# Performance work log

Hardware: AMD Instinct MI355X
Metric: run time of the kernel (lower is better)

The kernel has to match this reference:

```python
import jax, jax.numpy as jnp
import numpy as np
import math

N_HEADS = 16
FACTOR = 5
EPS = 1e-5


def layernorm(x, g, b):
    m = x.mean(-1, keepdims=True)
    v = x.var(-1, keepdims=True)
    return (x - m) / jnp.sqrt(v + EPS) * g + b


def prob_attention(Q, K, V, mask_flag, key):
    # Q: [B, L_Q, H, D], K/V: [B, L_K, H, D] -> internal [B, H, L, D] (Informer ProbAttention)
    Q = Q.transpose(0, 2, 1, 3)
    K = K.transpose(0, 2, 1, 3)
    V = V.transpose(0, 2, 1, 3)
    B, H, L_Q, D = Q.shape
    L_K = K.shape[2]
    U_part = min(FACTOR * int(np.ceil(np.log(L_K))), L_K)  # sampled keys per query
    u = min(FACTOR * int(np.ceil(np.log(L_Q))), L_Q)       # number of active queries
    # sample U_part key indices per query (shared over B, H as in Informer)
    idx = jax.random.randint(key, (L_Q, U_part), 0, L_K)
    K_s = K[:, :, idx, :]                                   # [B,H,L_Q,U_part,D]
    QKs = jnp.einsum('bhld,bhlsd->bhls', Q, K_s)            # sampled scores
    M = QKs.max(-1) - QKs.sum(-1) / L_K                     # sparsity measurement [B,H,L_Q]
    M_top = jax.lax.top_k(M, u)[1]                          # [B,H,u] active query indices
    Q_r = jnp.take_along_axis(Q, M_top[..., None], axis=2)  # [B,H,u,D]
    scale = 1.0 / math.sqrt(D)
    scores = jnp.einsum('bhud,bhkd->bhuk', Q_r, K) * scale  # [B,H,u,L_K]
    if mask_flag:
        # causal mask relative to each selected query's position
        causal = jnp.arange(L_K)[None, None, None, :] > M_top[..., None]
        scores = jnp.where(causal, -jnp.inf, scores)
        context = jnp.cumsum(V, axis=2)                     # initial context for masked case
    else:
        context = jnp.broadcast_to(V.mean(axis=2, keepdims=True), (B, H, L_Q, D))
    attn = jax.nn.softmax(scores, axis=-1)
    ctx = jnp.einsum('bhuk,bhkd->bhud', attn, V)            # [B,H,u,D]
    bi = jnp.arange(B)[:, None, None]
    hi = jnp.arange(H)[None, :, None]
    context = context.at[bi, hi, M_top].set(ctx)            # scatter active queries
    return context.transpose(0, 2, 1, 3)                    # [B,L_Q,H,D]


def mha(x, kv, Wq, bq, Wk, bk, Wv, bv, Wo, bo, mask_flag, key):
    B, L, Dm = x.shape
    Lc = kv.shape[1]
    Dh = Dm // N_HEADS
    Q = (x @ Wq + bq).reshape(B, L, N_HEADS, Dh)
    K = (kv @ Wk + bk).reshape(B, Lc, N_HEADS, Dh)
    V = (kv @ Wv + bv).reshape(B, Lc, N_HEADS, Dh)
    out = prob_attention(Q, K, V, mask_flag, key).reshape(B, L, Dm)
    return out @ Wo + bo


def forward(x, enc_out, sa_Wq, sa_bq, sa_Wk, sa_bk, sa_Wv, sa_bv, sa_Wo, sa_bo,
            ca_Wq, ca_bq, ca_Wk, ca_bk, ca_Wv, ca_bv, ca_Wo, ca_bo,
            ln1_g, ln1_b, ln2_g, ln2_b, ln3_g, ln3_b, ff_W1, ff_b1, ff_W2, ff_b2):
    k1, k2 = jax.random.split(jax.random.key(42))
    x2 = mha(x, x, sa_Wq, sa_bq, sa_Wk, sa_bk, sa_Wv, sa_bv, sa_Wo, sa_bo, True, k1)
    x = layernorm(x + x2, ln1_g, ln1_b)
    x2 = mha(x, enc_out, ca_Wq, ca_bq, ca_Wk, ca_bk, ca_Wv, ca_bv, ca_Wo, ca_bo, False, k2)
    x = layernorm(x + x2, ln2_g, ln2_b)
    x2 = (jax.nn.relu(x @ ff_W1 + ff_b1)) @ ff_W2 + ff_b2
    return layernorm(x + x2, ln3_g, ln3_b)


def setup_inputs() -> dict:
    key = jax.random.key(0)
    D, F = 1024, 4096
    B, L = 4, 1024
    ks = jax.random.split(key, 16)
    s = 0.02
    inp = {
        'x': jax.random.normal(ks[0], (B, L, D), jnp.float32),
        'enc_out': jax.random.normal(ks[1], (B, L, D), jnp.float32),
    }
    names = ['sa_Wq', 'sa_Wk', 'sa_Wv', 'sa_Wo', 'ca_Wq', 'ca_Wk', 'ca_Wv', 'ca_Wo']
    for i, n in enumerate(names):
        inp[n] = jax.random.normal(ks[2 + i], (D, D), jnp.float32) * s
        inp[n.replace('W', 'b')] = jnp.zeros((D,), jnp.float32)
    inp['ff_W1'] = jax.random.normal(ks[10], (D, F), jnp.float32) * s
    inp['ff_b1'] = jnp.zeros((F,), jnp.float32)
    inp['ff_W2'] = jax.random.normal(ks[11], (F, D), jnp.float32) * s
    inp['ff_b2'] = jnp.zeros((D,), jnp.float32)
    for i in (1, 2, 3):
        inp[f'ln{i}_g'] = jnp.ones((D,), jnp.float32)
        inp[f'ln{i}_b'] = jnp.zeros((D,), jnp.float32)
    return inp


def reference(x, enc_out, sa_Wq, sa_bq, sa_Wk, sa_bk, sa_Wv, sa_bv, sa_Wo, sa_bo,
              ca_Wq, ca_bq, ca_Wk, ca_bk, ca_Wv, ca_bv, ca_Wo, ca_bo,
              ln1_g, ln1_b, ln2_g, ln2_b, ln3_g, ln3_b, ff_W1, ff_b1, ff_W2, ff_b2):
    return forward(x, enc_out, sa_Wq, sa_bq, sa_Wk, sa_bk, sa_Wv, sa_bv, sa_Wo, sa_bo,
                   ca_Wq, ca_bq, ca_Wk, ca_bk, ca_Wv, ca_bv, ca_Wo, ca_bo,
                   ln1_g, ln1_b, ln2_g, ln2_b, ln3_g, ln3_b, ff_W1, ff_b1, ff_W2, ff_b2)
```

## Files before the change

kernel.cpp:

```cpp
#include <hip/hip_runtime.h>
#include <cstdint>
#include <cstddef>

#define B_     4
#define L_     1024
#define DM_    1024
#define H_     16
#define DH_    64
#define U_     35
#define FF_    4096
#define MROWS_ 4096
#define IDXN_  35840
#define KSC_   16
#define KSP_   16

typedef __attribute__((ext_vector_type(8))) short bf16x8;
typedef __attribute__((ext_vector_type(4))) float f32x4;

__host__ __device__ inline void tf2x32(uint32_t k0, uint32_t k1,
                                       uint32_t x0, uint32_t x1,
                                       uint32_t& y0, uint32_t& y1) {
  const uint32_t ks2 = k0 ^ k1 ^ 0x1BD11BDAu;
  uint32_t v0 = x0 + k0, v1 = x1 + k1;
#define ROTL_(x,d) (((x)<<(d))|((x)>>(32-(d))))
#define RND_(r) { v0 += v1; v1 = ROTL_(v1,(r)); v1 ^= v0; }
  RND_(13) RND_(15) RND_(26) RND_(6)   v0 += k1;  v1 += ks2 + 1u;
  RND_(17) RND_(29) RND_(16) RND_(24)  v0 += ks2; v1 += k0  + 2u;
  RND_(13) RND_(15) RND_(26) RND_(6)   v0 += k0;  v1 += k1  + 3u;
  RND_(17) RND_(29) RND_(16) RND_(24)  v0 += k1;  v1 += ks2 + 4u;
  RND_(13) RND_(15) RND_(26) RND_(6)   v0 += ks2; v1 += k0  + 5u;
#undef RND_
#undef ROTL_
  y0 = v0; y1 = v1;
}

__global__ void idx_kernel(uint32_t k0, uint32_t k1, int* __restrict__ idx) {
  const int i = blockIdx.x * 256 + threadIdx.x;
  if (i >= IDXN_) return;
  uint32_t y0, y1;
  tf2x32(k0, k1, 0u, (uint32_t)i, y0, y1);
  idx[i] = (int)((y0 ^ y1) & 1023u);
}

__device__ __forceinline__ uint32_t f32bits(float x) {
  union { float f; uint32_t u; } c; c.f = x; return c.u;
}
__device__ __forceinline__ float bitsf32(uint32_t u) {
  union { uint32_t u; float f; } c; c.u = u; return c.f;
}
__device__ __forceinline__ uint32_t bf16rne(float x) {
  const uint32_t u = f32bits(x);
  return (u + 0x7FFFu + ((u >> 16) & 1u)) >> 16;
}
__device__ __forceinline__ float bf16tof(uint32_t h) { return bitsf32(h << 16); }

__device__ __forceinline__ void split3(float x, uint32_t& h, uint32_t& m, uint32_t& l) {
  h = bf16rne(x); const float r  = x - bf16tof(h);
  m = bf16rne(r); const float r2 = r - bf16tof(m);
  l = bf16rne(r2);
}

__device__ __forceinline__ void gload16(const void* g, void* l) {
  __builtin_amdgcn_global_load_lds(
      (const __attribute__((address_space(1))) void*)g,
      (__attribute__((address_space(3))) void*)l, 16, 0, 0);
}

struct TSJob { const float* W; short* Th; short* Tm; short* Tl; int K; int N; int limbs; int nblk; };
struct TSJobs { TSJob j[4]; int cnt; };

__global__ __launch_bounds__(256) void tsplit_batch(TSJobs jobs)
{
  __shared__ float tile[64][65];
  int local = blockIdx.x;
  int ji = 0;
  while (ji < jobs.cnt - 1 && local >= jobs.j[ji].nblk) { local -= jobs.j[ji].nblk; ++ji; }
  const TSJob J = jobs.j[ji];
  const int ntiles = J.N >> 6;
  const int n0 = (local % ntiles) * 64;
  const int k0 = (local / ntiles) * 64;

  const int t = threadIdx.x;
  const int r = t >> 2, c0 = (t & 3) * 16;
  const float* src = J.W + (size_t)(k0 + r) * J.N + n0 + c0;
  const float4 v0 = *(const float4*)src;
  const float4 v1 = *(const float4*)(src + 4);
  const float4 v2 = *(const float4*)(src + 8);
  const float4 v3 = *(const float4*)(src + 12);
  float* tr = &tile[r][c0];
  tr[0]=v0.x; tr[1]=v0.y; tr[2]=v0.z; tr[3]=v0.w;
  tr[4]=v1.x; tr[5]=v1.y; tr[6]=v1.z; tr[7]=v1.w;
  tr[8]=v2.x; tr[9]=v2.y; tr[10]=v2.z; tr[11]=v2.w;
  tr[12]=v3.x; tr[13]=v3.y; tr[14]=v3.z; tr[15]=v3.w;
  __syncthreads();
  uint32_t ph[8], pm[8], pl[8];
#pragma unroll
  for (int j = 0; j < 16; j += 2) {
    uint32_t h0,m0,l0,h1,m1,l1;
    split3(tile[c0 + j][r], h0, m0, l0);
    split3(tile[c0 + j + 1][r], h1, m1, l1);
    ph[j>>1] = h0 | (h1 << 16);
    pm[j>>1] = m0 | (m1 << 16);
    pl[j>>1] = l0 | (l1 << 16);
  }
  const size_t ob = (size_t)(n0 + r) * J.K + k0 + c0;
  *(uint4*)(J.Th + ob)     = make_uint4(ph[0], ph[1], ph[2], ph[3]);
  *(uint4*)(J.Th + ob + 8) = make_uint4(ph[4], ph[5], ph[6], ph[7]);
  if (J.limbs == 3) {
    *(uint4*)(J.Tm + ob)     = make_uint4(pm[0], pm[1], pm[2], pm[3]);
    *(uint4*)(J.Tm + ob + 8) = make_uint4(pm[4], pm[5], pm[6], pm[7]);
    *(uint4*)(J.Tl + ob)     = make_uint4(pl[0], pl[1], pl[2], pl[3]);
    *(uint4*)(J.Tl + ob + 8) = make_uint4(pl[4], pl[5], pl[6], pl[7]);
  }
}

template<int LIMBS>
__global__ void rsplit_kernel(const float* __restrict__ X, short* __restrict__ Th,
                              short* __restrict__ Tm, short* __restrict__ Tl, int n8)
{
  const int i = blockIdx.x * 256 + threadIdx.x;
  if (i >= n8) return;
  const float4 a = ((const float4*)X)[2*i], b = ((const float4*)X)[2*i+1];
  const float v[8] = {a.x,a.y,a.z,a.w,b.x,b.y,b.z,b.w};
  uint32_t ph[4], pm[4], pl[4];
#pragma unroll
  for (int j = 0; j < 4; ++j) {
    uint32_t h0,m0,l0,h1,m1,l1;
    split3(v[2*j], h0, m0, l0);
    split3(v[2*j+1], h1, m1, l1);
    ph[j] = h0 | (h1 << 16); pm[j] = m0 | (m1 << 16); pl[j] = l0 | (l1 << 16);
  }
  ((uint4*)Th)[i] = make_uint4(ph[0], ph[1], ph[2], ph[3]);
  if (LIMBS == 3) {
    ((uint4*)Tm)[i] = make_uint4(pm[0], pm[1], pm[2], pm[3]);
    ((uint4*)Tl)[i] = make_uint4(pl[0], pl[1], pl[2], pl[3]);
  }
}

struct FJob {
  const short* A[3];
  const short* B[3];
  const float* bias;
  float* C;
  short* Ch;
  int relu;
};
struct FJobs { FJob j[3]; };

template<int NL>
__global__ __launch_bounds__(256, 3) void gemm_fused(FJobs jobs, int K, int N)
{
  __shared__ short As[NL][4096] __attribute__((aligned(16)));
  __shared__ short Bs[NL][4096] __attribute__((aligned(16)));
  const int z = blockIdx.z;
  const int nwg  = gridDim.x * gridDim.y;
  const int flat = blockIdx.y * gridDim.x + blockIdx.x;
  const int swz  = (flat & 7) * (nwg >> 3) + (flat >> 3);
  const int bn = (swz % gridDim.x) * 128;
  const int bm = (swz / gridDim.x) * 128;

  const int t = threadIdx.x, lane = t & 63;
  const int wid = t >> 6, wr = wid >> 1, wc = wid & 1;
  const int l15 = lane & 15, kg = lane >> 4;
  const int srow = t >> 2;
  const int sc   = ((t & 3) ^ ((srow + (srow >> 2)) & 3)) * 8;

  int aoff[4], boff[4];
#pragma unroll
  for (int m = 0; m < 4; ++m) {
    const int ra = wr * 64 + m * 16 + l15;
    aoff[m] = ra * 32 + ((kg ^ ((ra + (ra >> 2)) & 3)) << 3);
    const int rb = wc * 64 + m * 16 + l15;
    boff[m] = rb * 32 + ((kg ^ ((rb + (rb >> 2)) & 3)) << 3);
  }

  f32x4 acc[4][4];
#pragma unroll
  for (int m = 0; m < 4; ++m)
#pragma unroll
    for (int n = 0; n < 4; ++n) acc[m][n] = (f32x4){0.f,0.f,0.f,0.f};

  const size_t aofs0 = (size_t)(bm + srow) * K + sc;
  const size_t bofs0 = (size_t)(bn + srow) * K + sc;
  const size_t half  = (size_t)64 * K;

  for (int kk = 0; kk < K; kk += 32) {
    __syncthreads();
#pragma unroll
    for (int l = 0; l < NL; ++l) {
      gload16(jobs.j[z].A[l] + aofs0 + kk,        &As[l][t * 8]);
      gload16(jobs.j[z].A[l] + aofs0 + half + kk, &As[l][2048 + t * 8]);
      gload16(jobs.j[z].B[l] + bofs0 + kk,        &Bs[l][t * 8]);
      gload16(jobs.j[z].B[l] + bofs0 + half + kk, &Bs[l][2048 + t * 8]);
    }
    __syncthreads();
    if (NL == 1) {
      bf16x8 a[4], b[4];
#pragma unroll
      for (int m = 0; m < 4; ++m) a[m] = *(const bf16x8*)&As[0][aoff[m]];
#pragma unroll
      for (int n = 0; n < 4; ++n) b[n] = *(const bf16x8*)&Bs[0][boff[n]];
#pragma unroll
      for (int m = 0; m < 4; ++m)
#pragma unroll
        for (int n = 0; n < 4; ++n)
          acc[m][n] = __builtin_amdgcn_mfma_f32_16x16x32_bf16(a[m], b[n], acc[m][n], 0, 0, 0);
    } else {
      bf16x8 a0[4], a1[4], a2[4], b[4];
#pragma unroll
      for (int m = 0; m < 4; ++m) {
        a0[m] = *(const bf16x8*)&As[0][aoff[m]];
        a1[m] = *(const bf16x8*)&As[1][aoff[m]];
        a2[m] = *(const bf16x8*)&As[2][aoff[m]];
      }
#pragma unroll
      for (int n = 0; n < 4; ++n) b[n] = *(const bf16x8*)&Bs[0][boff[n]];
#pragma unroll
      for (int m = 0; m < 4; ++m)
#pragma unroll
        for (int n = 0; n < 4; ++n) {
          acc[m][n] = __builtin_amdgcn_mfma_f32_16x16x32_bf16(a0[m], b[n], acc[m][n], 0, 0, 0);
          acc[m][n] = __builtin_amdgcn_mfma_f32_16x16x32_bf16(a1[m], b[n], acc[m][n], 0, 0, 0);
          acc[m][n] = __builtin_amdgcn_mfma_f32_16x16x32_bf16(a2[m], b[n], acc[m][n], 0, 0, 0);
        }
#pragma unroll
      for (int n = 0; n < 4; ++n) b[n] = *(const bf16x8*)&Bs[1][boff[n]];
#pragma unroll
      for (int m = 0; m < 4; ++m)
#pragma unroll
        for (int n = 0; n < 4; ++n) {
          acc[m][n] = __builtin_amdgcn_mfma_f32_16x16x32_bf16(a0[m], b[n], acc[m][n], 0, 0, 0);
          acc[m][n] = __builtin_amdgcn_mfma_f32_16x16x32_bf16(a1[m], b[n], acc[m][n], 0, 0, 0);
        }
#pragma unroll
      for (int n = 0; n < 4; ++n) b[n] = *(const bf16x8*)&Bs[2][boff[n]];
#pragma unroll
      for (int m = 0; m < 4; ++m)
#pragma unroll
        for (int n = 0; n < 4; ++n)
          acc[m][n] = __builtin_amdgcn_mfma_f32_16x16x32_bf16(a0[m], b[n], acc[m][n], 0, 0, 0);
    }
  }

  const float* bias = jobs.j[z].bias;
  float* C  = jobs.j[z].C;
  short* Ch = jobs.j[z].Ch;
  const int relu = jobs.j[z].relu;
  float bv[4];
#pragma unroll
  for (int n = 0; n < 4; ++n) bv[n] = bias[bn + wc*64 + n*16 + l15];
#pragma unroll
  for (int m = 0; m < 4; ++m) {
    const int row0 = bm + wr*64 + m*16 + kg*4;
#pragma unroll
    for (int n = 0; n < 4; ++n) {
      const int col = bn + wc*64 + n*16 + l15;
#pragma unroll
      for (int q = 0; q < 4; ++q) {
        float o = acc[m][n][q] + bv[n];
        if (relu) o = fmaxf(o, 0.f);
        const size_t off = (size_t)(row0 + q) * N + col;
        if (C)  C[off]  = o;
        if (Ch) Ch[off] = (short)bf16rne(o);
      }
    }
  }
}

__global__ __launch_bounds__(256, 3) void gemm_one(FJob job, int K, int N)
{
  __shared__ short As[2][4096] __attribute__((aligned(16)));
  __shared__ short Bs[2][4096] __attribute__((aligned(16)));
  const int nwg  = gridDim.x * gridDim.y;
  const int flat = blockIdx.y * gridDim.x + blockIdx.x;
  const int swz  = (flat & 7) * (nwg >> 3) + (flat >> 3);
  const int bn = (swz % gridDim.x) * 128;
  const int bm = (swz / gridDim.x) * 128;

  const int t = threadIdx.x, lane = t & 63;
  const int wid = t >> 6, wr = wid >> 1, wc = wid & 1;
  const int l15 = lane & 15, kg = lane >> 4;
  const int srow = t >> 2;
  const int sc   = ((t & 3) ^ ((srow + (srow >> 2)) & 3)) * 8;

  int aoff[4], boff[4];
#pragma unroll
  for (int m = 0; m < 4; ++m) {
    const int ra = wr * 64 + m * 16 + l15;
    aoff[m] = ra * 32 + ((kg ^ ((ra + (ra >> 2)) & 3)) << 3);
    const int rb = wc * 64 + m * 16 + l15;
    boff[m] = rb * 32 + ((kg ^ ((rb + (rb >> 2)) & 3)) << 3);
  }

  f32x4 acc[4][4];
#pragma unroll
  for (int m = 0; m < 4; ++m)
#pragma unroll
    for (int n = 0; n < 4; ++n) acc[m][n] = (f32x4){0.f,0.f,0.f,0.f};

  const size_t aofs0 = (size_t)(bm + srow) * K + sc;
  const size_t bofs0 = (size_t)(bn + srow) * K + sc;
  const size_t half  = (size_t)64 * K;

  gload16(job.A[0] + aofs0,        &As[0][t * 8]);
  gload16(job.A[0] + aofs0 + half, &As[0][2048 + t * 8]);
  gload16(job.B[0] + bofs0,        &Bs[0][t * 8]);
  gload16(job.B[0] + bofs0 + half, &Bs[0][2048 + t * 8]);
  __syncthreads();

  int cur = 0;
  for (int kk = 0; kk < K; kk += 32) {
    const int nxt = kk + 32;
    if (nxt < K) {
      const int nb = cur ^ 1;
      gload16(job.A[0] + aofs0 + nxt,        &As[nb][t * 8]);
      gload16(job.A[0] + aofs0 + half + nxt, &As[nb][2048 + t * 8]);
      gload16(job.B[0] + bofs0 + nxt,        &Bs[nb][t * 8]);
      gload16(job.B[0] + bofs0 + half + nxt, &Bs[nb][2048 + t * 8]);
    }
    bf16x8 a[4], b[4];
#pragma unroll
    for (int m = 0; m < 4; ++m) a[m] = *(const bf16x8*)&As[cur][aoff[m]];
#pragma unroll
    for (int n = 0; n < 4; ++n) b[n] = *(const bf16x8*)&Bs[cur][boff[n]];
#pragma unroll
    for (int m = 0; m < 4; ++m)
#pragma unroll
      for (int n = 0; n < 4; ++n)
        acc[m][n] = __builtin_amdgcn_mfma_f32_16x16x32_bf16(a[m], b[n], acc[m][n], 0, 0, 0);
    __syncthreads();
    cur ^= 1;
  }

  const float* bias = job.bias;
  float* C  = job.C;
  short* Ch = job.Ch;
  const int relu = job.relu;
  float bv[4];
#pragma unroll
  for (int n = 0; n < 4; ++n) bv[n] = bias[bn + wc*64 + n*16 + l15];
#pragma unroll
  for (int m = 0; m < 4; ++m) {
    const int row0 = bm + wr*64 + m*16 + kg*4;
#pragma unroll
    for (int n = 0; n < 4; ++n) {
      const int col = bn + wc*64 + n*16 + l15;
#pragma unroll
      for (int q = 0; q < 4; ++q) {
        float o = acc[m][n][q] + bv[n];
        if (relu) o = fmaxf(o, 0.f);
        const size_t off = (size_t)(row0 + q) * N + col;
        if (C)  C[off]  = o;
        if (Ch) Ch[off] = (short)bf16rne(o);
      }
    }
  }
}

__global__ __launch_bounds__(256, 2) void qks_m_kernel(
    const float* __restrict__ Q, const float* __restrict__ K,
    const int* __restrict__ idx, float* __restrict__ Mout)
{
  __shared__ int sidx[64 * U_];
  const int p = blockIdx.x;
  const int g  = (p & 7) + (((p >> 3) & 7) << 3);
  const int q16 = p >> 6;
  const int l0 = q16 * 64;
  const int tid = threadIdx.x;
  for (int i = tid; i < 64 * U_; i += 256) sidx[i] = idx[l0 * U_ + i];
  __syncthreads();

  const int ll = tid >> 2, dq = tid & 3;
  const int l = l0 + ll;
  const int h = g & (H_ - 1), b = g >> 4;
  const size_t rowb = (size_t)(b * L_) * DM_ + h * DH_;
  const float* qrow = Q + rowb + (size_t)l * DM_ + dq * 4;
  float4 qv[4];
#pragma unroll
  for (int jj = 0; jj < 4; ++jj) qv[jj] = *(const float4*)(qrow + jj * 16);

  const int* ip = &sidx[ll * U_];
  float mx = -__builtin_inff();
  float sm = 0.f;
#pragma unroll 5
  for (int s = 0; s < U_; ++s) {
    const float* krow = K + rowb + (size_t)ip[s] * DM_ + dq * 4;
    const float4 k0 = *(const float4*)(krow);
    const float4 k1 = *(const float4*)(krow + 16);
    const float4 k2 = *(const float4*)(krow + 32);
    const float4 k3 = *(const float4*)(krow + 48);
    float a0 = 0.f, a1 = 0.f, a2 = 0.f, a3 = 0.f;
    a0 = fmaf(qv[0].x, k0.x, a0); a0 = fmaf(qv[0].y, k0.y, a0);
    a0 = fmaf(qv[0].z, k0.z, a0); a0 = fmaf(qv[0].w, k0.w, a0);
    a1 = fmaf(qv[1].x, k1.x, a1); a1 = fmaf(qv[1].y, k1.y, a1);
    a1 = fmaf(qv[1].z, k1.z, a1); a1 = fmaf(qv[1].w, k1.w, a1);
    a2 = fmaf(qv[2].x, k2.x, a2); a2 = fmaf(qv[2].y, k2.y, a2);
    a2 = fmaf(qv[2].z, k2.z, a2); a2 = fmaf(qv[2].w, k2.w, a2);
    a3 = fmaf(qv[3].x, k3.x, a3); a3 = fmaf(qv[3].y, k3.y, a3);
    a3 = fmaf(qv[3].z, k3.z, a3); a3 = fmaf(qv[3].w, k3.w, a3);
    float a = (a0 + a1) + (a2 + a3);
    a += __shfl_xor(a, 1, 64);
    a += __shfl_xor(a, 2, 64);
    mx = fmaxf(mx, a);
    sm += a;
  }
  if (dq == 0) Mout[g * L_ + l] = mx - sm * (1.0f / 1024.0f);
}

__global__ __launch_bounds__(256) void topk_kernel(
    const float* __restrict__ M, int* __restrict__ Mtop)
{
  const int bh  = blockIdx.x;
  const int tid = threadIdx.x;
  __shared__ float vals[L_];
  __shared__ float rv[256];
  __shared__ int   ri[256];
  for (int i = tid; i < L_; i += 256) vals[i] = M[(size_t)bh * L_ + i];
  __syncthreads();
  for (int t = 0; t < U_; ++t) {
    float best = -__builtin_inff();
    int   bi   = L_;
    for (int i = tid; i < L_; i += 256) {
      const float v = vals[i];
      if (v > best) { best = v; bi = i; }
    }
    rv[tid] = best; ri[tid] = bi;
    __syncthreads();
    for (int s = 128; s > 0; s >>= 1) {
      if (tid < s) {
        if (rv[tid+s] > rv[tid] || (rv[tid+s] == rv[tid] && ri[tid+s] < ri[tid])) {
          rv[tid] = rv[tid+s]; ri[tid] = ri[tid+s];
        }
      }
      __syncthreads();
    }
    if (tid == 0) { Mtop[bh * U_ + t] = ri[0]; vals[ri[0]] = -__builtin_inff(); }
    __syncthreads();
  }
}

__global__ __launch_bounds__(256) void attn_score(
    const float* __restrict__ Q, const float* __restrict__ K,
    const int* __restrict__ Mtop, uint32_t* __restrict__ Pg, int masked)
{
  __shared__ float qs[U_ * DH_];
  __shared__ int   rowsL[U_ + 1];
  const int p = blockIdx.x;
  const int xcd = p & 7, idx2 = p >> 3;
  const int bh = xcd + ((idx2 & 7) << 3);
  const int ks = idx2 >> 3;
  const int h = bh & (H_ - 1), b = bh >> 4;
  const int tid = threadIdx.x;
  const size_t kvbase = (size_t)(b * L_) * DM_ + h * DH_;

  if (tid < U_) rowsL[tid] = Mtop[bh * U_ + tid];
  __syncthreads();
  for (int i = tid; i < U_ * DH_; i += 256)
    qs[i] = Q[kvbase + (size_t)rowsL[i >> 6] * DM_ + (i & 63)];
  __syncthreads();

  const int grp = tid >> 2, dq = tid & 3;
  const int k = ks * 64 + grp;
  const float* kp = K + kvbase + (size_t)k * DM_ + dq * 16;
  const float4 kv0 = *(const float4*)(kp);
  const float4 kv1 = *(const float4*)(kp + 4);
  const float4 kv2 = *(const float4*)(kp + 8);
  const float4 kv3 = *(const float4*)(kp + 12);

#define DOT_EXP_U(uu, out)                                                  \
  {                                                                         \
    const float4* qp = (const float4*)&qs[(uu) * 64 + dq * 16];             \
    const float4 q0 = qp[0], q1 = qp[1], q2 = qp[2], q3 = qp[3];            \
    float x0 = 0.f, x1 = 0.f;                                               \
    x0 = fmaf(q0.x, kv0.x, x0); x0 = fmaf(q0.y, kv0.y, x0);                 \
    x0 = fmaf(q0.z, kv0.z, x0); x0 = fmaf(q0.w, kv0.w, x0);                 \
    x1 = fmaf(q1.x, kv1.x, x1); x1 = fmaf(q1.y, kv1.y, x1);                 \
    x1 = fmaf(q1.z, kv1.z, x1); x1 = fmaf(q1.w, kv1.w, x1);                 \
    x0 = fmaf(q2.x, kv2.x, x0); x0 = fmaf(q2.y, kv2.y, x0);                 \
    x0 = fmaf(q2.z, kv2.z, x0); x0 = fmaf(q2.w, kv2.w, x0);                 \
    x1 = fmaf(q3.x, kv3.x, x1); x1 = fmaf(q3.y, kv3.y, x1);                 \
    x1 = fmaf(q3.z, kv3.z, x1); x1 = fmaf(q3.w, kv3.w, x1);                 \
    float a = x0 + x1;                                                      \
    a += __shfl_xor(a, 1, 64);                                              \
    a += __shfl_xor(a, 2, 64);                                              \
    float v = a * 0.125f;                                                   \
    if (masked && k > rowsL[(uu)]) v = -__builtin_inff();                   \
    out = expf(v);                                                          \
  }

  uint32_t pk[18];
#pragma unroll
  for (int j = 0; j < 17; ++j) {
    float e0, e1;
    DOT_EXP_U(2 * j, e0);
    DOT_EXP_U(2 * j + 1, e1);
    pk[j] = bf16rne(e0) | (bf16rne(e1) << 16);
  }
  {
    float e;
    DOT_EXP_U(34, e);
    pk[17] = bf16rne(e);
  }
#undef DOT_EXP_U

  if (dq == 0) {
    uint32_t* prow = Pg + (size_t)bh * (L_ * 18) + (size_t)k * 18;
#pragma unroll
    for (int j = 0; j < 18; ++j) prow[j] = pk[j];
  }
}

__global__ __launch_bounds__(256) void attn_pv(
    const float* __restrict__ V, const uint32_t* __restrict__ Pg,
    float* __restrict__ Opart, float* __restrict__ Dpart)
{
  __shared__ uint32_t Pl[64 * 18];
  const int p = blockIdx.x;
  const int xcd = p & 7, idx2 = p >> 3;
  const int bh = xcd + ((idx2 & 7) << 3);
  const int ks = idx2 >> 3;
  const int h = bh & (H_ - 1), b = bh >> 4;
  const int tid = threadIdx.x, lane = tid & 63, wid = tid >> 6;
  const size_t kvbase = (size_t)(b * L_) * DM_ + h * DH_;

  const uint32_t* ps = Pg + (size_t)bh * (L_ * 18) + (size_t)(ks * 64) * 18;
  for (int i = tid; i < 64 * 18; i += 256) Pl[i] = ps[i];
  __syncthreads();

  float acc[9], dd[9];
#pragma unroll
  for (int j = 0; j < 9; ++j) { acc[j] = 0.f; dd[j] = 0.f; }

  const float* vp = V + kvbase + (size_t)(ks * 64) * DM_ + lane;
  const int widh = wid >> 1;
  const int hi   = wid & 1;
#pragma unroll 8
  for (int kk = 0; kk < 64; ++kk) {
    const float v0 = vp[(size_t)kk * DM_];
    const uint32_t* pr = &Pl[kk * 18];
#pragma unroll
    for (int j = 0; j < 9; ++j) {
      if (wid + 4 * j < U_) {
        const uint32_t w = pr[widh + 2 * j];
        const float p2 = hi ? bitsf32(w & 0xFFFF0000u) : bitsf32(w << 16);
        acc[j] = fmaf(p2, v0, acc[j]);
        dd[j] += p2;
      }
    }
  }
  const int pb = (ks * 64 + bh) * U_;
#pragma unroll
  for (int j = 0; j < 9; ++j) {
    const int u = wid + 4 * j;
    if (u < U_) {
      Opart[(size_t)(pb + u) * 64 + lane] = acc[j];
      if (lane == 0) Dpart[pb + u] = dd[j];
    }
  }
}

__global__ void attn_reduce(const float* __restrict__ Opart,
                            const float* __restrict__ Dpart,
                            float* __restrict__ ctx_rows)
{
  const int bhu = blockIdx.x;
  const int bh = bhu / U_, u = bhu % U_;
  const int lane = threadIdx.x;
  float o = 0.f, dd = 0.f;
#pragma unroll
  for (int ks = 0; ks < KSP_; ++ks) {
    o  += Opart[(size_t)((ks * 64 + bh) * U_ + u) * 64 + lane];
    dd += Dpart[(ks * 64 + bh) * U_ + u];
  }
  ctx_rows[(size_t)bhu * 64 + lane] = o / dd;
}

__global__ __launch_bounds__(256) void cumsum_kernel(
    const float* __restrict__ V, float* __restrict__ C)
{
  const int bh = blockIdx.x;
  const int h = bh & (H_ - 1), b = bh >> 4;
  const int d = threadIdx.x & 63, qq = threadIdx.x >> 6;
  __shared__ float chs[4][DH_];
  const size_t base = (size_t)b * L_ * DM_ + h * DH_ + d;
  float acc = 0.f;
  const int l0 = qq * 256;
  for (int l = l0; l < l0 + 256; ++l) acc += V[base + (size_t)l * DM_];
  chs[qq][d] = acc;
  __syncthreads();
  float off = 0.f;
  for (int j = 0; j < qq; ++j) off += chs[j][d];
  acc = off;
  for (int l = l0; l < l0 + 256; ++l) {
    acc += V[base + (size_t)l * DM_];
    C[base + (size_t)l * DM_] = acc;
  }
}

__global__ __launch_bounds__(256) void vmean_kernel(
    const float* __restrict__ V, float* __restrict__ vm)
{
  const int bh = blockIdx.x;
  const int h = bh & (H_ - 1), b = bh >> 4;
  const int d = threadIdx.x & 63, qq = threadIdx.x >> 6;
  __shared__ float chs[4][DH_];
  const size_t base = (size_t)b * L_ * DM_ + h * DH_ + d;
  float acc = 0.f;
  for (int l = qq * 256; l < qq * 256 + 256; ++l) acc += V[base + (size_t)l * DM_];
  chs[qq][d] = acc;
  __syncthreads();
  if (qq == 0)
    vm[bh * DH_ + d] = (chs[0][d] + chs[1][d] + chs[2][d] + chs[3][d]) * (1.0f / 1024.0f);
}

__global__ void fill_kernel(const float* __restrict__ vm, float* __restrict__ C)
{
  const size_t i = (size_t)blockIdx.x * 256 + threadIdx.x;
  const int d = (int)(i & 63);
  const int h = (int)((i >> 6) & (H_ - 1));
  const int b = (int)(i >> 20);
  C[i] = vm[(b * H_ + h) * DH_ + d];
}

__global__ void scatter_kernel(const float* __restrict__ ctx_rows,
                               const int* __restrict__ Mtop, float* __restrict__ C)
{
  const int bhu = blockIdx.x;
  const int u  = bhu % U_;
  const int bh = bhu / U_;
  const int h = bh & (H_ - 1), b = bh >> 4;
  const int row = Mtop[bh * U_ + u];
  C[(size_t)(b * L_ + row) * DM_ + h * DH_ + threadIdx.x] =
      ctx_rows[(size_t)bhu * DH_ + threadIdx.x];
}

__global__ __launch_bounds__(256) void ln_kernel(
    const float* __restrict__ xa, const float* __restrict__ xb,
    const float* __restrict__ g, const float* __restrict__ bt,
    float* __restrict__ out, short* __restrict__ oh,
    short* __restrict__ om, short* __restrict__ ol)
{
  const int row = blockIdx.x;
  const int tid = threadIdx.x;
  __shared__ float v[DM_];
  __shared__ float red[256];
  float s = 0.f;
  for (int i = tid; i < DM_; i += 256) {
    const float t = xa[(size_t)row * DM_ + i] + xb[(size_t)row * DM_ + i];
    v[i] = t; s += t;
  }
  red[tid] = s; __syncthreads();
  for (int st = 128; st > 0; st >>= 1) { if (tid < st) red[tid] += red[tid+st]; __syncthreads(); }
  const float mean = red[0] * (1.0f / DM_);
  __syncthreads();
  float s2 = 0.f;
  for (int i = tid; i < DM_; i += 256) { const float dd = v[i] - mean; s2 += dd * dd; }
  red[tid] = s2; __syncthreads();
  for (int st = 128; st > 0; st >>= 1) { if (tid < st) red[tid] += red[tid+st]; __syncthreads(); }
  const float rstd = rsqrtf(red[0] * (1.0f / DM_) + 1e-5f);
  __syncthreads();
  for (int i = tid; i < DM_; i += 256) {
    const size_t idx = (size_t)row * DM_ + i;
    const float o = (v[i] - mean) * rstd * g[i] + bt[i];
    out[idx] = o;
    if (oh) {
      const uint32_t h = bf16rne(o);
      oh[idx] = (short)h;
      if (om) {
        const float r = o - bf16tof(h);
        const uint32_t m = bf16rne(r);
        om[idx] = (short)m;
        ol[idx] = (short)bf16rne(r - bf16tof(m));
      }
    }
  }
}

extern "C" void kernel_launch(void* const* d_in, const int* in_sizes, int n_in,
                              void* d_out, int out_size, void* d_ws, size_t ws_size,
                              hipStream_t stream)
{
  (void)in_sizes; (void)n_in; (void)out_size; (void)ws_size;
  const float* x    = (const float*)d_in[0];
  const float* enc  = (const float*)d_in[1];
  const float* saWq = (const float*)d_in[2];  const float* sabq = (const float*)d_in[3];
  const float* saWk = (const float*)d_in[4];  const float* sabk = (const float*)d_in[5];
  const float* saWv = (const float*)d_in[6];  const float* sabv = (const float*)d_in[7];
  const float* saWo = (const float*)d_in[8];  const float* sabo = (const float*)d_in[9];
  const float* caWq = (const float*)d_in[10]; const float* cabq = (const float*)d_in[11];
  const float* caWk = (const float*)d_in[12]; const float* cabk = (const float*)d_in[13];
  const float* caWv = (const float*)d_in[14]; const float* cabv = (const float*)d_in[15];
  const float* caWo = (const float*)d_in[16]; const float* cabo = (const float*)d_in[17];
  const float* fW1  = (const float*)d_in[18]; const float* fb1  = (const float*)d_in[19];
  const float* fW2  = (const float*)d_in[20]; const float* fb2  = (const float*)d_in[21];
  const float* l1g  = (const float*)d_in[22]; const float* l1b  = (const float*)d_in[23];
  const float* l2g  = (const float*)d_in[24]; const float* l2b  = (const float*)d_in[25];
  const float* l3g  = (const float*)d_in[26]; const float* l3b  = (const float*)d_in[27];

  float* ws = (float*)d_ws;
  const size_t SL = (size_t)MROWS_ * DM_;
  float* bufQ = ws;
  float* bufK = ws + SL;
  float* bufV = ws + 2 * SL;
  float* bufC = ws + 3 * SL;
  float* xcur = ws + 4 * SL;
  float* tmp  = ws + 5 * SL;
  float* smallp = ws + 6 * SL;
  int*   idxb = (int*)smallp;
  float* Mbuf = smallp + 36864;
  int*   Mtop = (int*)(smallp + 36864 + 65536);
  float* ctxr = smallp + 36864 + 65536 + 2304;
  float* vm   = ctxr + 143360;

  uint32_t* Pg    = (uint32_t*)bufC;
  float*    Opart = bufC + 1179648;
  float*    Dpart = Opart + (size_t)KSP_ * 64 * U_ * 64;

  const size_t M1 = 1024u * 1024u;
  short* wreg = (short*)(ws + 6 * SL + 262144);
  short* areg = wreg + 8 * M1;
  short* Wqh = wreg;          short* Wqm = wreg + 1*M1; short* Wql = wreg + 2*M1;
  short* Wkh = wreg + 3*M1;   short* Wkm = wreg + 4*M1; short* Wkl = wreg + 5*M1;
  short* Wvh = wreg + 6*M1;   short* Woh = wreg + 7*M1;
  short* f1h = wreg;          short* f2h = wreg + 4*M1;
  short* xh = areg;           short* xm = areg + 4*M1;  short* xl = areg + 8*M1;
  short* eh = areg + 12*M1;   short* em = areg + 16*M1; short* el = areg + 20*M1;
  short* bCh = areg + 12*M1;
  short* hidh = (short*)bufQ;

  uint32_t k1a, k1b, k2a, k2b;
  tf2x32(0u, 42u, 0u, 0u, k1a, k1b);
  tf2x32(0u, 42u, 0u, 1u, k2a, k2b);
  uint32_t kb1a, kb1b, kb2a, kb2b;
  tf2x32(k1a, k1b, 0u, 1u, kb1a, kb1b);
  tf2x32(k2a, k2b, 0u, 1u, kb2a, kb2b);

  const dim3 thr(256);
  const int gIdx = (IDXN_ + 255) / 256;
  const int n8 = (int)(SL / 8);

  const dim3 gP1(DM_ / 128, MROWS_ / 128, 1);
  const dim3 gP2(DM_ / 128, MROWS_ / 128, 2);
  const dim3 gF1(FF_ / 128, MROWS_ / 128, 1);

  {
    TSJobs T = {};
    T.j[0] = { saWq, Wqh, Wqm, Wql, DM_, DM_, 3, 256 };
    T.j[1] = { saWk, Wkh, Wkm, Wkl, DM_, DM_, 3, 256 };
    T.j[2] = { saWv, Wvh, nullptr, nullptr, DM_, DM_, 1, 256 };
    T.j[3] = { saWo, Woh, nullptr, nullptr, DM_, DM_, 1, 256 };
    T.cnt = 4;
    tsplit_batch<<<1024, thr, 0, stream>>>(T);
  }
  rsplit_kernel<3><<<n8 / 256, thr, 0, stream>>>(x, xh, xm, xl, n8);
  {
    FJobs J = {};
    J.j[0] = { {xh, xm, xl}, {Wqh, Wqm, Wql}, sabq, bufQ, nullptr, 0 };
    J.j[1] = { {xh, xm, xl}, {Wkh, Wkm, Wkl}, sabk, bufK, nullptr, 0 };
    gemm_fused<3><<<gP2, thr, 0, stream>>>(J, DM_, DM_);
  }
  {
    FJob J = { {xh, nullptr, nullptr}, {Wvh, nullptr, nullptr}, sabv, bufV, nullptr, 0 };
    gemm_one<<<gP1, thr, 0, stream>>>(J, DM_, DM_);
  }
  idx_kernel<<<gIdx, thr, 0, stream>>>(kb1a, kb1b, idxb);
  qks_m_kernel<<<1024, thr, 0, stream>>>(bufQ, bufK, idxb, Mbuf);
  topk_kernel<<<B_ * H_, thr, 0, stream>>>(Mbuf, Mtop);
  attn_score<<<B_ * H_ * KSC_, thr, 0, stream>>>(bufQ, bufK, Mtop, Pg, 1);
  attn_pv<<<B_ * H_ * KSP_, thr, 0, stream>>>(bufV, Pg, Opart, Dpart);
  attn_reduce<<<B_ * H_ * U_, dim3(64), 0, stream>>>(Opart, Dpart, ctxr);
  cumsum_kernel<<<B_ * H_, thr, 0, stream>>>(bufV, bufC);
  scatter_kernel<<<B_ * H_ * U_, dim3(64), 0, stream>>>(ctxr, Mtop, bufC);
  rsplit_kernel<1><<<n8 / 256, thr, 0, stream>>>(bufC, bCh, nullptr, nullptr, n8);
  {
    FJob J = { {bCh, nullptr, nullptr}, {Woh, nullptr, nullptr}, sabo, tmp, nullptr, 0 };
    gemm_one<<<gP1, thr, 0, stream>>>(J, DM_, DM_);
  }
  ln_kernel<<<MROWS_, thr, 0, stream>>>(x, tmp, l1g, l1b, xcur, xh, xm, xl);

  {
    TSJobs T = {};
    T.j[0] = { caWq, Wqh, Wqm, Wql, DM_, DM_, 3, 256 };
    T.j[1] = { caWk, Wkh, Wkm, Wkl, DM_, DM_, 3, 256 };
    T.j[2] = { caWv, Wvh, nullptr, nullptr, DM_, DM_, 1, 256 };
    T.j[3] = { caWo, Woh, nullptr, nullptr, DM_, DM_, 1, 256 };
    T.cnt = 4;
    tsplit_batch<<<1024, thr, 0, stream>>>(T);
  }
  rsplit_kernel<3><<<n8 / 256, thr, 0, stream>>>(enc, eh, em, el, n8);
  {
    FJobs J = {};
    J.j[0] = { {xh, xm, xl}, {Wqh, Wqm, Wql}, cabq, bufQ, nullptr, 0 };
    J.j[1] = { {eh, em, el}, {Wkh, Wkm, Wkl}, cabk, bufK, nullptr, 0 };
    gemm_fused<3><<<gP2, thr, 0, stream>>>(J, DM_, DM_);
  }
  {
    FJob J = { {eh, nullptr, nullptr}, {Wvh, nullptr, nullptr}, cabv, bufV, nullptr, 0 };
    gemm_one<<<gP1, thr, 0, stream>>>(J, DM_, DM_);
  }
  idx_kernel<<<gIdx, thr, 0, stream>>>(kb2a, kb2b, idxb);
  qks_m_kernel<<<1024, thr, 0, stream>>>(bufQ, bufK, idxb, Mbuf);
  topk_kernel<<<B_ * H_, thr, 0, stream>>>(Mbuf, Mtop);
  attn_score<<<B_ * H_ * KSC_, thr, 0, stream>>>(bufQ, bufK, Mtop, Pg, 0);
  attn_pv<<<B_ * H_ * KSP_, thr, 0, stream>>>(bufV, Pg, Opart, Dpart);
  attn_reduce<<<B_ * H_ * U_, dim3(64), 0, stream>>>(Opart, Dpart, ctxr);
  vmean_kernel<<<B_ * H_, thr, 0, stream>>>(bufV, vm);
  fill_kernel<<<(int)(SL / 256), thr, 0, stream>>>(vm, bufC);
  scatter_kernel<<<B_ * H_ * U_, dim3(64), 0, stream>>>(ctxr, Mtop, bufC);
  rsplit_kernel<1><<<n8 / 256, thr, 0, stream>>>(bufC, bCh, nullptr, nullptr, n8);
  {
    FJob J = { {bCh, nullptr, nullptr}, {Woh, nullptr, nullptr}, cabo, tmp, nullptr, 0 };
    gemm_one<<<gP1, thr, 0, stream>>>(J, DM_, DM_);
  }
  ln_kernel<<<MROWS_, thr, 0, stream>>>(xcur, tmp, l2g, l2b, xcur, xh, nullptr, nullptr);

  {
    TSJobs T = {};
    T.j[0] = { fW1, f1h, nullptr, nullptr, DM_, FF_, 1, 1024 };
    T.j[1] = { fW2, f2h, nullptr, nullptr, FF_, DM_, 1, 1024 };
    T.cnt = 2;
    tsplit_batch<<<2048, thr, 0, stream>>>(T);
  }
  {
    FJob J = { {xh, nullptr, nullptr}, {f1h, nullptr, nullptr}, fb1, nullptr, hidh, 1 };
    gemm_one<<<gF1, thr, 0, stream>>>(J, DM_, FF_);
  }
  {
    FJob J = { {hidh, nullptr, nullptr}, {f2h, nullptr, nullptr}, fb2, tmp, nullptr, 0 };
    gemm_one<<<gP1, thr, 0, stream>>>(J, FF_, DM_);
  }
  ln_kernel<<<MROWS_, thr, 0, stream>>>(xcur, tmp, l3g, l3b, (float*)d_out,
                                        nullptr, nullptr, nullptr);
}
```

Before: 774.1 us.

## Split-K the 3-limb Q/K projection GEMM and use wave-shuffle top-k reduction

The fused 3-limb Q/K projection GEMM is replaced by a split-K version that gives each of Q and K three K-ranges, launching 6x the 256 tiles instead of 2x. A separate combine kernel sums the fp32 partials and adds the bias. The aim is to fill the GPU better, since only 512 workgroups ran before. In exchange it adds roughly 100 MB of extra partial-sum traffic and one more launch. Top-k now reduces with wavefront shuffles instead of an 8-step shared-memory tree full of barriers.

Result: slower. 792.2 us (+2.3%).

```diff
diff --git a/kernel.cpp b/kernel.cpp
--- a/kernel.cpp
+++ b/kernel.cpp
@@ -137,6 +137,135 @@
   }
 }
 
+struct QKJob { const short* A[3]; const short* B[3]; float* P; int kbeg; int kend; };
+struct QKJobs { QKJob j[6]; };
+
+__global__ __launch_bounds__(256, 3) void gemm_qk(QKJobs jobs, int K, int N)
+{
+  __shared__ short As[3][4096] __attribute__((aligned(16)));
+  __shared__ short Bs[3][4096] __attribute__((aligned(16)));
+  const int z = blockIdx.z;
+  const int nwg  = gridDim.x * gridDim.y;
+  const int flat = blockIdx.y * gridDim.x + blockIdx.x;
+  const int swz  = (flat & 7) * (nwg >> 3) + (flat >> 3);
+  const int bn = (swz % gridDim.x) * 128;
+  const int bm = (swz / gridDim.x) * 128;
+
+  const int t = threadIdx.x, lane = t & 63;
+  const int wid = t >> 6, wr = wid >> 1, wc = wid & 1;
+  const int l15 = lane & 15, kg = lane >> 4;
+  const int srow = t >> 2;
+  const int sc   = ((t & 3) ^ ((srow + (srow >> 2)) & 3)) * 8;
+
+  int aoff[4], boff[4];
+#pragma unroll
+  for (int m = 0; m < 4; ++m) {
+    const int ra = wr * 64 + m * 16 + l15;
+    aoff[m] = ra * 32 + ((kg ^ ((ra + (ra >> 2)) & 3)) << 3);
+    const int rb = wc * 64 + m * 16 + l15;
+    boff[m] = rb * 32 + ((kg ^ ((rb + (rb >> 2)) & 3)) << 3);
+  }
+
+  f32x4 acc[4][4];
+#pragma unroll
+  for (int m = 0; m < 4; ++m)
+#pragma unroll
+    for (int n = 0; n < 4; ++n) acc[m][n] = (f32x4){0.f,0.f,0.f,0.f};
+
+  const size_t aofs0 = (size_t)(bm + srow) * K + sc;
+  const size_t bofs0 = (size_t)(bn + srow) * K + sc;
+  const size_t half  = (size_t)64 * K;
+
+  const int kbeg = jobs.j[z].kbeg, kend = jobs.j[z].kend;
+  for (int kk = kbeg; kk < kend; kk += 32) {
+    __syncthreads();
+#pragma unroll
+    for (int l = 0; l < 3; ++l) {
+      gload16(jobs.j[z].A[l] + aofs0 + kk,        &As[l][t * 8]);
+      gload16(jobs.j[z].A[l] + aofs0 + half + kk, &As[l][2048 + t * 8]);
+      gload16(jobs.j[z].B[l] + bofs0 + kk,        &Bs[l][t * 8]);
+      gload16(jobs.j[z].B[l] + bofs0 + half + kk, &Bs[l][2048 + t * 8]);
+    }
+    __syncthreads();
+    bf16x8 a0[4], a1[4], a2[4], b[4];
+#pragma unroll
+    for (int m = 0; m < 4; ++m) {
+      a0[m] = *(const bf16x8*)&As[0][aoff[m]];
+      a1[m] = *(const bf16x8*)&As[1][aoff[m]];
+      a2[m] = *(const bf16x8*)&As[2][aoff[m]];
+    }
+#pragma unroll
+    for (int n = 0; n < 4; ++n) b[n] = *(const bf16x8*)&Bs[0][boff[n]];
+#pragma unroll
+    for (int m = 0; m < 4; ++m)
+#pragma unroll
+      for (int n = 0; n < 4; ++n) {
+        acc[m][n] = __builtin_amdgcn_mfma_f32_16x16x32_bf16(a0[m], b[n], acc[m][n], 0, 0, 0);
+        acc[m][n] = __builtin_amdgcn_mfma_f32_16x16x32_bf16(a1[m], b[n], acc[m][n], 0, 0, 0);
+        acc[m][n] = __builtin_amdgcn_mfma_f32_16x16x32_bf16(a2[m], b[n], acc[m][n], 0, 0, 0);
+      }
+#pragma unroll
+    for (int n = 0; n < 4; ++n) b[n] = *(const bf16x8*)&Bs[1][boff[n]];
+#pragma unroll
+    for (int m = 0; m < 4; ++m)
+#pragma unroll
+      for (int n = 0; n < 4; ++n) {
+        acc[m][n] = __builtin_amdgcn_mfma_f32_16x16x32_bf16(a0[m], b[n], acc[m][n], 0, 0, 0);
+        acc[m][n] = __builtin_amdgcn_mfma_f32_16x16x32_bf16(a1[m], b[n], acc[m][n], 0, 0, 0);
+      }
+#pragma unroll
+    for (int n = 0; n < 4; ++n) b[n] = *(const bf16x8*)&Bs[2][boff[n]];
+#pragma unroll
+    for (int m = 0; m < 4; ++m)
+#pragma unroll
+      for (int n = 0; n < 4; ++n)
+        acc[m][n] = __builtin_amdgcn_mfma_f32_16x16x32_bf16(a0[m], b[n], acc[m][n], 0, 0, 0);
+  }
+
+  float* P = jobs.j[z].P;
+#pragma unroll
+  for (int m = 0; m < 4; ++m) {
+    const int row0 = bm + wr*64 + m*16 + kg*4;
+#pragma unroll
+    for (int n = 0; n < 4; ++n) {
+      const int col = bn + wc*64 + n*16 + l15;
+#pragma unroll
+      for (int q = 0; q < 4; ++q)
+        P[(size_t)(row0 + q) * N + col] = acc[m][n][q];
+    }
+  }
+}
+
+__global__ void qk_combine(const float* q0, const float* q1, const float* q2,
+                           const float* bq, float* Qo,
+                           const float* k0, const float* k1, const float* k2,
+                           const float* bk, float* Ko)
+{
+  const size_t i = ((size_t)blockIdx.x * 256 + threadIdx.x) * 8;
+  const int col = (int)(i & (DM_ - 1));
+#define CMB8_(p0, p1, p2, bb, oo)                                            \
+  {                                                                          \
+    const float4 x0 = *(const float4*)((p0) + i);                            \
+    const float4 x1 = *(const float4*)((p1) + i);                            \
+    const float4 x2 = *(const float4*)((p2) + i);                            \
+    const float4 y0 = *(const float4*)((p0) + i + 4);                        \
+    const float4 y1 = *(const float4*)((p1) + i + 4);                        \
+    const float4 y2 = *(const float4*)((p2) + i + 4);                        \
+    const float4 b0 = *(const float4*)((bb) + col);                          \
+    const float4 b1 = *(const float4*)((bb) + col + 4);                      \
+    float4 r0, r1;                                                           \
+    r0.x = x0.x + x1.x + x2.x + b0.x; r0.y = x0.y + x1.y + x2.y + b0.y;      \
+    r0.z = x0.z + x1.z + x2.z + b0.z; r0.w = x0.w + x1.w + x2.w + b0.w;      \
+    r1.x = y0.x + y1.x + y2.x + b1.x; r1.y = y0.y + y1.y + y2.y + b1.y;      \
+    r1.z = y0.z + y1.z + y2.z + b1.z; r1.w = y0.w + y1.w + y2.w + b1.w;      \
+    *(float4*)((oo) + i) = r0;                                               \
+    *(float4*)((oo) + i + 4) = r1;                                           \
+  }
+  CMB8_(q0, q1, q2, bq, Qo)
+  CMB8_(k0, k1, k2, bk, Ko)
+#undef CMB8_
+}
+
 struct FJob {
   const short* A[3];
   const short* B[3];
@@ -145,127 +274,6 @@
   short* Ch;
   int relu;
 };
-struct FJobs { FJob j[3]; };
-
-template<int NL>
-__global__ __launch_bounds__(256, 3) void gemm_fused(FJobs jobs, int K, int N)
-{
-  __shared__ short As[NL][4096] __attribute__((aligned(16)));
-  __shared__ short Bs[NL][4096] __attribute__((aligned(16)));
-  const int z = blockIdx.z;
-  const int nwg  = gridDim.x * gridDim.y;
-  const int flat = blockIdx.y * gridDim.x + blockIdx.x;
-  const int swz  = (flat & 7) * (nwg >> 3) + (flat >> 3);
-  const int bn = (swz % gridDim.x) * 128;
-  const int bm = (swz / gridDim.x) * 128;
-
-  const int t = threadIdx.x, lane = t & 63;
-  const int wid = t >> 6, wr = wid >> 1, wc = wid & 1;
-  const int l15 = lane & 15, kg = lane >> 4;
-  const int srow = t >> 2;
-  const int sc   = ((t & 3) ^ ((srow + (srow >> 2)) & 3)) * 8;
-
-  int aoff[4], boff[4];
-#pragma unroll
-  for (int m = 0; m < 4; ++m) {
-    const int ra = wr * 64 + m * 16 + l15;
-    aoff[m] = ra * 32 + ((kg ^ ((ra + (ra >> 2)) & 3)) << 3);
-    const int rb = wc * 64 + m * 16 + l15;
-    boff[m] = rb * 32 + ((kg ^ ((rb + (rb >> 2)) & 3)) << 3);
-  }
-
-  f32x4 acc[4][4];
-#pragma unroll
-  for (int m = 0; m < 4; ++m)
-#pragma unroll
-    for (int n = 0; n < 4; ++n) acc[m][n] = (f32x4){0.f,0.f,0.f,0.f};
-
-  const size_t aofs0 = (size_t)(bm + srow) * K + sc;
-  const size_t bofs0 = (size_t)(bn + srow) * K + sc;
-  const size_t half  = (size_t)64 * K;
-
-  for (int kk = 0; kk < K; kk += 32) {
-    __syncthreads();
-#pragma unroll
-    for (int l = 0; l < NL; ++l) {
-      gload16(jobs.j[z].A[l] + aofs0 + kk,        &As[l][t * 8]);
-      gload16(jobs.j[z].A[l] + aofs0 + half + kk, &As[l][2048 + t * 8]);
-      gload16(jobs.j[z].B[l] + bofs0 + kk,        &Bs[l][t * 8]);
-      gload16(jobs.j[z].B[l] + bofs0 + half + kk, &Bs[l][2048 + t * 8]);
-    }
-    __syncthreads();
-    if (NL == 1) {
-      bf16x8 a[4], b[4];
-#pragma unroll
-      for (int m = 0; m < 4; ++m) a[m] = *(const bf16x8*)&As[0][aoff[m]];
-#pragma unroll
-      for (int n = 0; n < 4; ++n) b[n] = *(const bf16x8*)&Bs[0][boff[n]];
-#pragma unroll
-      for (int m = 0; m < 4; ++m)
-#pragma unroll
-        for (int n = 0; n < 4; ++n)
-          acc[m][n] = __builtin_amdgcn_mfma_f32_16x16x32_bf16(a[m], b[n], acc[m][n], 0, 0, 0);
-    } else {
-      bf16x8 a0[4], a1[4], a2[4], b[4];
-#pragma unroll
-      for (int m = 0; m < 4; ++m) {
-        a0[m] = *(const bf16x8*)&As[0][aoff[m]];
-        a1[m] = *(const bf16x8*)&As[1][aoff[m]];
-        a2[m] = *(const bf16x8*)&As[2][aoff[m]];
-      }
-#pragma unroll
-      for (int n = 0; n < 4; ++n) b[n] = *(const bf16x8*)&Bs[0][boff[n]];
-#pragma unroll
-      for (int m = 0; m < 4; ++m)
-#pragma unroll
-        for (int n = 0; n < 4; ++n) {
-          acc[m][n] = __builtin_amdgcn_mfma_f32_16x16x32_bf16(a0[m], b[n], acc[m][n], 0, 0, 0);
-          acc[m][n] = __builtin_amdgcn_mfma_f32_16x16x32_bf16(a1[m], b[n], acc[m][n], 0, 0, 0);
-          acc[m][n] = __builtin_amdgcn_mfma_f32_16x16x32_bf16(a2[m], b[n], acc[m][n], 0, 0, 0);
-        }
-#pragma unroll
-      for (int n = 0; n < 4; ++n) b[n] = *(const bf16x8*)&Bs[1][boff[n]];
-#pragma unroll
-      for (int m = 0; m < 4; ++m)
-#pragma unroll
-        for (int n = 0; n < 4; ++n) {
-          acc[m][n] = __builtin_amdgcn_mfma_f32_16x16x32_bf16(a0[m], b[n], acc[m][n], 0, 0, 0);
-          acc[m][n] = __builtin_amdgcn_mfma_f32_16x16x32_bf16(a1[m], b[n], acc[m][n], 0, 0, 0);
-        }
-#pragma unroll
-      for (int n = 0; n < 4; ++n) b[n] = *(const bf16x8*)&Bs[2][boff[n]];
-#pragma unroll
-      for (int m = 0; m < 4; ++m)
-#pragma unroll
-        for (int n = 0; n < 4; ++n)
-          acc[m][n] = __builtin_amdgcn_mfma_f32_16x16x32_bf16(a0[m], b[n], acc[m][n], 0, 0, 0);
-    }
-  }
-
-  const float* bias = jobs.j[z].bias;
-  float* C  = jobs.j[z].C;
-  short* Ch = jobs.j[z].Ch;
-  const int relu = jobs.j[z].relu;
-  float bv[4];
-#pragma unroll
-  for (int n = 0; n < 4; ++n) bv[n] = bias[bn + wc*64 + n*16 + l15];
-#pragma unroll
-  for (int m = 0; m < 4; ++m) {
-    const int row0 = bm + wr*64 + m*16 + kg*4;
-#pragma unroll
-    for (int n = 0; n < 4; ++n) {
-      const int col = bn + wc*64 + n*16 + l15;
-#pragma unroll
-      for (int q = 0; q < 4; ++q) {
-        float o = acc[m][n][q] + bv[n];
-        if (relu) o = fmaxf(o, 0.f);
-        const size_t off = (size_t)(row0 + q) * N + col;
-        if (C)  C[off]  = o;
-        if (Ch) Ch[off] = (short)bf16rne(o);
-      }
-    }
-  }
-}
 
 __global__ __launch_bounds__(256, 3) void gemm_one(FJob job, int K, int N)
 {
@@ -412,9 +420,10 @@
 {
   const int bh  = blockIdx.x;
   const int tid = threadIdx.x;
+  const int lane = tid & 63, wv = tid >> 6;
   __shared__ float vals[L_];
-  __shared__ float rv[256];
-  __shared__ int   ri[256];
+  __shared__ float rv[4];
+  __shared__ int   ri[4];
   for (int i = tid; i < L_; i += 256) vals[i] = M[(size_t)bh * L_ + i];
   __syncthreads();
   for (int t = 0; t < U_; ++t) {
@@ -424,17 +433,22 @@
       const float v = vals[i];
       if (v > best) { best = v; bi = i; }
     }
-    rv[tid] = best; ri[tid] = bi;
+#pragma unroll
+    for (int d = 1; d < 64; d <<= 1) {
+      const float ov = __shfl_xor(best, d, 64);
+      const int   oi = __shfl_xor(bi, d, 64);
+      if (ov > best || (ov == best && oi < bi)) { best = ov; bi = oi; }
+    }
+    if (lane == 0) { rv[wv] = best; ri[wv] = bi; }
     __syncthreads();
-    for (int s = 128; s > 0; s >>= 1) {
-      if (tid < s) {
-        if (rv[tid+s] > rv[tid] || (rv[tid+s] == rv[tid] && ri[tid+s] < ri[tid])) {
-          rv[tid] = rv[tid+s]; ri[tid] = ri[tid+s];
-        }
-      }
-      __syncthreads();
-    }
-    if (tid == 0) { Mtop[bh * U_ + t] = ri[0]; vals[ri[0]] = -__builtin_inff(); }
+    if (tid == 0) {
+      float bb = rv[0]; int bj = ri[0];
+#pragma unroll
+      for (int w = 1; w < 4; ++w)
+        if (rv[w] > bb || (rv[w] == bb && ri[w] < bj)) { bb = rv[w]; bj = ri[w]; }
+      Mtop[bh * U_ + t] = bj;
+      vals[bj] = -__builtin_inff();
+    }
     __syncthreads();
   }
 }
@@ -727,6 +741,7 @@
   short* eh = areg + 12*M1;   short* em = areg + 16*M1; short* el = areg + 20*M1;
   short* bCh = areg + 12*M1;
   short* hidh = (short*)bufQ;
+  float* extra = (float*)(areg + 24 * M1);
 
   uint32_t k1a, k1b, k2a, k2b;
   tf2x32(0u, 42u, 0u, 0u, k1a, k1b);
@@ -740,8 +755,9 @@
   const int n8 = (int)(SL / 8);
 
   const dim3 gP1(DM_ / 128, MROWS_ / 128, 1);
-  const dim3 gP2(DM_ / 128, MROWS_ / 128, 2);
+  const dim3 gQK(DM_ / 128, MROWS_ / 128, 6);
   const dim3 gF1(FF_ / 128, MROWS_ / 128, 1);
+  const int gCmb = (int)(SL / 8 / 256);
 
   {
     TSJobs T = {};
@@ -754,10 +770,16 @@
   }
   rsplit_kernel<3><<<n8 / 256, thr, 0, stream>>>(x, xh, xm, xl, n8);
   {
-    FJobs J = {};
-    J.j[0] = { {xh, xm, xl}, {Wqh, Wqm, Wql}, sabq, bufQ, nullptr, 0 };
-    J.j[1] = { {xh, xm, xl}, {Wkh, Wkm, Wkl}, sabk, bufK, nullptr, 0 };
-    gemm_fused<3><<<gP2, thr, 0, stream>>>(J, DM_, DM_);
+    QKJobs J = {};
+    J.j[0] = { {xh, xm, xl}, {Wqh, Wqm, Wql}, bufQ, 0, 352 };
+    J.j[1] = { {xh, xm, xl}, {Wqh, Wqm, Wql}, bufC, 352, 704 };
+    J.j[2] = { {xh, xm, xl}, {Wqh, Wqm, Wql}, xcur, 704, 1024 };
+    J.j[3] = { {xh, xm, xl}, {Wkh, Wkm, Wkl}, bufK, 0, 352 };
+    J.j[4] = { {xh, xm, xl}, {Wkh, Wkm, Wkl}, bufV, 352, 704 };
+    J.j[5] = { {xh, xm, xl}, {Wkh, Wkm, Wkl}, tmp, 704, 1024 };
+    gemm_qk<<<gQK, thr, 0, stream>>>(J, DM_, DM_);
+    qk_combine<<<gCmb, thr, 0, stream>>>(bufQ, bufC, xcur, sabq, bufQ,
+                                         bufK, bufV, tmp, sabk, bufK);
   }
   {
     FJob J = { {xh, nullptr, nullptr}, {Wvh, nullptr, nullptr}, sabv, bufV, nullptr, 0 };
@@ -789,10 +811,16 @@
   }
   rsplit_kernel<3><<<n8 / 256, thr, 0, stream>>>(enc, eh, em, el, n8);
   {
-    FJobs J = {};
-    J.j[0] = { {xh, xm, xl}, {Wqh, Wqm, Wql}, cabq, bufQ, nullptr, 0 };
-    J.j[1] = { {eh, em, el}, {Wkh, Wkm, Wkl}, cabk, bufK, nullptr, 0 };
-    gemm_fused<3><<<gP2, thr, 0, stream>>>(J, DM_, DM_);
+    QKJobs J = {};
+    J.j[0] = { {xh, xm, xl}, {Wqh, Wqm, Wql}, bufQ, 0, 352 };
+    J.j[1] = { {xh, xm, xl}, {Wqh, Wqm, Wql}, bufC, 352, 704 };
+    J.j[2] = { {xh, xm, xl}, {Wqh, Wqm, Wql}, extra, 704, 1024 };
+    J.j[3] = { {eh, em, el}, {Wkh, Wkm, Wkl}, bufK, 0, 352 };
+    J.j[4] = { {eh, em, el}, {Wkh, Wkm, Wkl}, bufV, 352, 704 };
+    J.j[5] = { {eh, em, el}, {Wkh, Wkm, Wkl}, tmp, 704, 1024 };
+    gemm_qk<<<gQK, thr, 0, stream>>>(J, DM_, DM_);
+    qk_combine<<<gCmb, thr, 0, stream>>>(bufQ, bufC, extra, cabq, bufQ,
+                                         bufK, bufV, tmp, cabk, bufK);
   }
   {
     FJob J = { {eh, nullptr, nullptr}, {Wvh, nullptr, nullptr}, cabv, bufV, nullptr, 0 };
```
